# Kernel tuning notes

Hardware: AMD Instinct MI355X
Metric: run time of the kernel (lower is better)

The kernel has to match this reference:

```python
import jax, jax.numpy as jnp
import numpy as np

D = 1024            # BIGNET_DIM
GS = 16             # group_size
NG = D * D // GS    # groups per layer = 65536
N_LAYERS = 18       # 6 blocks * 3 linears
LORA_LAYERS = {0: 0, 6: 1, 12: 2}  # linear index -> lora slot (first linear of blocks 0,2,4)
RANK = 32
BATCH = 16384
EPS = 1e-5


def setup_inputs() -> dict:
    key = jax.random.key(0)
    ks = jax.random.split(key, 6)
    x = jax.random.normal(ks[0], (BATCH, D), dtype=jnp.float32)
    w_q = jax.random.randint(ks[1], (N_LAYERS, NG, GS), 0, 16, dtype=jnp.int32)
    w_norm = jax.random.uniform(ks[2], (N_LAYERS, NG, 1), dtype=jnp.float32)
    bias = jax.random.normal(ks[3], (N_LAYERS, D), dtype=jnp.float32) * 0.02
    lora_a = jax.random.normal(ks[4], (3, RANK, D), dtype=jnp.float32) * (1.0 / np.sqrt(D))
    lora_b = jax.random.normal(ks[5], (3, D, RANK), dtype=jnp.float32) * 0.02
    ln_w = jnp.ones((6, D), dtype=jnp.float32)
    ln_b = jnp.zeros((6, D), dtype=jnp.float32)
    return {"x": x, "w_q": w_q, "w_norm": w_norm, "bias": bias,
            "lora_a": lora_a, "lora_b": lora_b, "ln_w": ln_w, "ln_b": ln_b}


def _dequant(q, n):
    # block_dequantize_4bit: codes in [0,15] -> [-norm, +norm] per group
    return ((q.astype(jnp.float32) / 15.0) * 2.0 - 1.0) * n  # [NG, GS]


def reference(x, w_q, w_norm, bias, lora_a, lora_b, ln_w, ln_b):
    h = x
    for blk in range(6):
        for pos in range(3):
            l = blk * 3 + pos
            W = _dequant(w_q[l], w_norm[l]).reshape(D, D)  # [out, in]
            out = h @ W.T + bias[l]
            if l in LORA_LAYERS:
                i = LORA_LAYERS[l]
                out = out + (h @ lora_a[i].T) @ lora_b[i].T
            if pos < 2:
                out = jax.nn.relu(out)
            h = out
        mu = jnp.mean(h, axis=-1, keepdims=True)
        var = jnp.mean(jnp.square(h - mu), axis=-1, keepdims=True)
        h = (h - mu) * jax.lax.rsqrt(var + EPS) * ln_w[blk] + ln_b[blk]
    return h
```

## Files before the change

kernel.cpp:

```cpp
#include <hip/hip_runtime.h>
#include <cstdint>
#include <cstddef>


typedef short  bf16x8 __attribute__((ext_vector_type(8)));
typedef float  f32x4  __attribute__((ext_vector_type(4)));

__device__ __forceinline__ unsigned short f2bf(float f) {
  unsigned int u = __builtin_bit_cast(unsigned int, f);
  u += 0x7FFFu + ((u >> 16) & 1u);
  return (unsigned short)(u >> 16);
}

__device__ __forceinline__ void async_copy16(void* lds, const void* g) {
  __builtin_amdgcn_global_load_lds(
      (const __attribute__((address_space(1))) void*)(uintptr_t)(g),
      (__attribute__((address_space(3))) void*)(unsigned int)(uintptr_t)(lds),
      16, 0, 0);
}

__global__ __launch_bounds__(256) void dequant_kernel(
    const int* __restrict__ wq, const float* __restrict__ wn,
    const float* __restrict__ lora_a, const float* __restrict__ lora_b,
    unsigned short* __restrict__ Wbf) {
  const int l   = blockIdx.y;
  const int t   = threadIdx.x;
  const int blk = blockIdx.x;
  const long base = (long)l * 1048576;
  const float s = 2.0f / 15.0f;

  int4  q[4];
  float nrm[4];
#pragma unroll
  for (int k = 0; k < 4; ++k) {
    const int i4 = blk * 1024 + k * 256 + t;
    q[k]   = *(const int4*)(wq + base + (long)i4 * 4);
    nrm[k] = wn[l * 65536 + (i4 >> 2)];
  }

  float v[4][4];
#pragma unroll
  for (int k = 0; k < 4; ++k) {
    v[k][0] = ((float)q[k].x * s - 1.0f) * nrm[k];
    v[k][1] = ((float)q[k].y * s - 1.0f) * nrm[k];
    v[k][2] = ((float)q[k].z * s - 1.0f) * nrm[k];
    v[k][3] = ((float)q[k].w * s - 1.0f) * nrm[k];
  }

  const int slot = (l == 0) ? 0 : (l == 6) ? 1 : (l == 12) ? 2 : -1;
  if (slot >= 0) {
    const float* A = lora_a + slot * 32768 + t * 4;
    const float* B = lora_b + slot * 32768 + blk * 128;
#pragma unroll 8
    for (int r = 0; r < 32; ++r) {
      const float4 a4 = *(const float4*)(A + r * 1024);
#pragma unroll
      for (int k = 0; k < 4; ++k) {
        const float br = B[k * 32 + r];
        v[k][0] = fmaf(br, a4.x, v[k][0]);
        v[k][1] = fmaf(br, a4.y, v[k][1]);
        v[k][2] = fmaf(br, a4.z, v[k][2]);
        v[k][3] = fmaf(br, a4.w, v[k][3]);
      }
    }
  }

#pragma unroll
  for (int k = 0; k < 4; ++k) {
    unsigned short u[4] = {f2bf(v[k][0]), f2bf(v[k][1]),
                           f2bf(v[k][2]), f2bf(v[k][3])};
    const long e0 = base + ((long)blk * 1024 + k * 256 + t) * 4;
    *(uint2*)(Wbf + e0) = *(uint2*)u;
  }
}

__global__ __launch_bounds__(256) void cvt_bf16_kernel(
    const float* __restrict__ in, unsigned short* __restrict__ out) {
  const long b0 = (long)blockIdx.x * 4096 + threadIdx.x * 4;
  float4 v[4];
#pragma unroll
  for (int k = 0; k < 4; ++k) v[k] = *(const float4*)(in + b0 + k * 1024);
#pragma unroll
  for (int k = 0; k < 4; ++k) {
    unsigned short u[4] = {f2bf(v[k].x), f2bf(v[k].y), f2bf(v[k].z), f2bf(v[k].w)};
    *(ushort4*)(out + b0 + k * 1024) = *(ushort4*)u;
  }
}

template <int MODE>
__global__ __launch_bounds__(256, 4) void gemm_kernel(
    const unsigned short* __restrict__ H,
    const unsigned short* __restrict__ W,
    const float* __restrict__ bias,
    unsigned short* __restrict__ outb,
    float* __restrict__ outf) {
  constexpr int K = 1024;
  constexpr int NN = 1024;

  __shared__ uint4 ldsq[2048];
  char* base = (char*)ldsq;

  const int tid = threadIdx.x;
  const int w   = tid >> 6;
  const int ln  = tid & 63;
  const int b   = blockIdx.x;
  const int m0  = ((b & 7) * 16 + (b >> 6)) * 128;
  const int n0  = ((b >> 3) & 7) * 128;

  const int gc = (ln & 7) ^ (ln >> 3);
  const unsigned short* gA = H + (size_t)(m0 + w * 32 + (ln >> 3)) * K + gc * 8;
  const unsigned short* gB = W + (size_t)(n0 + w * 32 + (ln >> 3)) * K + gc * 8;
  char* ldsA = base + w * 4096;
  char* ldsB = base + 16384 + w * 4096;

  const int quad = ln >> 4;
  const int lrow = ln & 15;
  const int sw   = lrow & 7;
  const int c0   = ((quad)     ^ sw) * 16;
  const int c1   = ((quad + 4) ^ sw) * 16;
  const int wm   = (w >> 1) * 64;
  const int wn   = (w & 1) * 64;
  const char* fragA = base + (wm + lrow) * 128;
  const char* fragB = base + 16384 + (wn + lrow) * 128;

  f32x4 acc[4][4];
#pragma unroll
  for (int i = 0; i < 4; ++i)
#pragma unroll
    for (int j = 0; j < 4; ++j) acc[i][j] = (f32x4){0.f, 0.f, 0.f, 0.f};

  for (int kt = 0; kt < 16; ++kt) {
    const unsigned short* pA = gA + kt * 64;
    const unsigned short* pB = gB + kt * 64;
#pragma unroll
    for (int i = 0; i < 4; ++i) {
      async_copy16(ldsA + i * 1024, pA + (size_t)i * 8 * K);
      async_copy16(ldsB + i * 1024, pB + (size_t)i * 8 * K);
    }
    __syncthreads();
#pragma unroll
    for (int kk = 0; kk < 2; ++kk) {
      const int co = kk ? c1 : c0;
      bf16x8 af[4], bg[4];
#pragma unroll
      for (int mt = 0; mt < 4; ++mt)
        af[mt] = *(const bf16x8*)(fragA + mt * 2048 + co);
#pragma unroll
      for (int nt = 0; nt < 4; ++nt)
        bg[nt] = *(const bf16x8*)(fragB + nt * 2048 + co);
#pragma unroll
      for (int mt = 0; mt < 4; ++mt)
#pragma unroll
        for (int nt = 0; nt < 4; ++nt)
          acc[mt][nt] = __builtin_amdgcn_mfma_f32_16x16x32_bf16(
              af[mt], bg[nt], acc[mt][nt], 0, 0, 0);
    }
    __syncthreads();
  }

#pragma unroll
  for (int nt = 0; nt < 4; ++nt) {
    const int n = n0 + wn + nt * 16 + lrow;
    const float bs = bias[n];
#pragma unroll
    for (int mt = 0; mt < 4; ++mt) {
      const int mb = m0 + wm + mt * 16 + quad * 4;
      f32x4 v = acc[mt][nt];
#pragma unroll
      for (int r = 0; r < 4; ++r) {
        float o = v[r] + bs;
        if (MODE == 0) {
          o = fmaxf(o, 0.0f);
          outb[(size_t)(mb + r) * NN + n] = f2bf(o);
        } else {
          outf[(size_t)(mb + r) * NN + n] = o;
        }
      }
    }
  }
}

__global__ __launch_bounds__(256) void ln_kernel(
    const float* __restrict__ in, const float* __restrict__ lnw,
    const float* __restrict__ lnb, unsigned short* __restrict__ outb,
    float* __restrict__ outf, int wf32) {
  const int wv = threadIdx.x >> 6;
  const int ln = threadIdx.x & 63;
  const int row = blockIdx.x * 4 + wv;
  const float* p = in + (size_t)row * 1024;

  float4 v[4];
  float s = 0.f, q = 0.f;
#pragma unroll
  for (int c = 0; c < 4; ++c) {
    v[c] = *(const float4*)(p + c * 256 + ln * 4);
    s += v[c].x + v[c].y + v[c].z + v[c].w;
    q += v[c].x * v[c].x + v[c].y * v[c].y + v[c].z * v[c].z + v[c].w * v[c].w;
  }
#pragma unroll
  for (int off = 32; off; off >>= 1) {
    s += __shfl_xor(s, off);
    q += __shfl_xor(q, off);
  }
  const float mu  = s * (1.0f / 1024.0f);
  const float var = q * (1.0f / 1024.0f) - mu * mu;
  const float rs  = rsqrtf(var + 1e-5f);

#pragma unroll
  for (int c = 0; c < 4; ++c) {
    const int col = c * 256 + ln * 4;
    const float4 w4 = *(const float4*)(lnw + col);
    const float4 b4 = *(const float4*)(lnb + col);
    const float y0 = (v[c].x - mu) * rs * w4.x + b4.x;
    const float y1 = (v[c].y - mu) * rs * w4.y + b4.y;
    const float y2 = (v[c].z - mu) * rs * w4.z + b4.z;
    const float y3 = (v[c].w - mu) * rs * w4.w + b4.w;
    unsigned short u[4] = {f2bf(y0), f2bf(y1), f2bf(y2), f2bf(y3)};
    *(ushort4*)(outb + (size_t)row * 1024 + col) = *(ushort4*)u;
    if (wf32) {
      float4 y = make_float4(y0, y1, y2, y3);
      *(float4*)(outf + (size_t)row * 1024 + col) = y;
    }
  }
}

extern "C" void kernel_launch(void* const* d_in, const int* in_sizes, int n_in,
                              void* d_out, int out_size, void* d_ws, size_t ws_size,
                              hipStream_t stream) {
  const float* x    = (const float*)d_in[0];
  const int*   wq   = (const int*)d_in[1];
  const float* wn   = (const float*)d_in[2];
  const float* bias = (const float*)d_in[3];
  const float* la   = (const float*)d_in[4];
  const float* lb   = (const float*)d_in[5];
  const float* lnw  = (const float*)d_in[6];
  const float* lnb  = (const float*)d_in[7];
  float* out = (float*)d_out;

  char* ws = (char*)d_ws;
  unsigned short* Wbf = (unsigned short*)ws;
  unsigned short* hA  = (unsigned short*)(ws + 37748736);
  unsigned short* hB  = (unsigned short*)(ws + 37748736 + 33554432);

  dequant_kernel<<<dim3(256, 18), 256, 0, stream>>>(wq, wn, la, lb, Wbf);
  cvt_bf16_kernel<<<4096, 256, 0, stream>>>(x, hA);

  for (int blk = 0; blk < 6; ++blk) {
    const int l = blk * 3;
    gemm_kernel<0><<<1024, 256, 0, stream>>>(
        hA, Wbf + (size_t)l * 1048576, bias + l * 1024, hB, nullptr);
    gemm_kernel<0><<<1024, 256, 0, stream>>>(
        hB, Wbf + (size_t)(l + 1) * 1048576, bias + (l + 1) * 1024, hA, nullptr);
    gemm_kernel<1><<<1024, 256, 0, stream>>>(
        hA, Wbf + (size_t)(l + 2) * 1048576, bias + (l + 2) * 1024, nullptr, out);
    ln_kernel<<<4096, 256, 0, stream>>>(
        out, lnw + blk * 1024, lnb + blk * 1024, hA, out, blk == 5 ? 1 : 0);
  }
}
```

Measured before the change: 968.6 us.

## Replace GEMM with 256x256-tile, 8-wave, double-buffered pipelined kernel

Rewrites the bf16 GEMM to use 256x256 output tiles per 512-thread block, with a 128KB dynamic LDS double buffer. Global-to-LDS async copies for the next K tiles are interleaved with MFMA sub-blocks, using explicit vmcnt/lgkmcnt waits, barriers and setprio. The aim is to hide memory latency and raise operand reuse per LDS load. In exchange it uses only 256 blocks, which may underfill the GPU's CUs, and it relies on hand-tuned waitcnt sequencing that is fragile.

```diff
diff --git a/kernel.cpp b/kernel.cpp
--- a/kernel.cpp
+++ b/kernel.cpp
@@ -88,92 +88,161 @@
 }
 
 template <int MODE>
-__global__ __launch_bounds__(256, 4) void gemm_kernel(
+__global__ __launch_bounds__(512, 2) void gemm8_kernel(
     const unsigned short* __restrict__ H,
     const unsigned short* __restrict__ W,
     const float* __restrict__ bias,
     unsigned short* __restrict__ outb,
     float* __restrict__ outf) {
-  constexpr int K = 1024;
-  constexpr int NN = 1024;
-
-  __shared__ uint4 ldsq[2048];
-  char* base = (char*)ldsq;
+  extern __shared__ char smem[];
 
   const int tid = threadIdx.x;
   const int w   = tid >> 6;
   const int ln  = tid & 63;
-  const int b   = blockIdx.x;
-  const int m0  = ((b & 7) * 16 + (b >> 6)) * 128;
-  const int n0  = ((b >> 3) & 7) * 128;
-
-  const int gc = (ln & 7) ^ (ln >> 3);
-  const unsigned short* gA = H + (size_t)(m0 + w * 32 + (ln >> 3)) * K + gc * 8;
-  const unsigned short* gB = W + (size_t)(n0 + w * 32 + (ln >> 3)) * K + gc * 8;
-  char* ldsA = base + w * 4096;
-  char* ldsB = base + 16384 + w * 4096;
+  const int wm  = w >> 2;
+  const int wn  = w & 3;
+
+  const int b  = blockIdx.x;
+  const int s  = (b & 7) * 32 + (b >> 3);
+  const int m0 = (s >> 2) * 256;
+  const int n0 = (s & 3) * 256;
+
+  const int gc    = (ln & 7) ^ ((ln >> 3) & 7);
+  const int rowst = w * 8 + (ln >> 3);
+  const unsigned eA = (unsigned)(m0 + rowst) * 1024u + gc * 8;
+  const unsigned eB = (unsigned)(n0 + rowst) * 1024u + gc * 8;
+  const int wofs = w * 1024;
 
   const int quad = ln >> 4;
   const int lrow = ln & 15;
   const int sw   = lrow & 7;
   const int c0   = ((quad)     ^ sw) * 16;
   const int c1   = ((quad + 4) ^ sw) * 16;
-  const int wm   = (w >> 1) * 64;
-  const int wn   = (w & 1) * 64;
-  const char* fragA = base + (wm + lrow) * 128;
-  const char* fragB = base + 16384 + (wn + lrow) * 128;
-
-  f32x4 acc[4][4];
-#pragma unroll
-  for (int i = 0; i < 4; ++i)
+  const int aoff = (wm * 128 + lrow) * 128;
+  const int boff = (wn * 64  + lrow) * 128;
+
+#define STAGE_A(T_, D_, F_, J_)                                                \
+  async_copy16(smem + (D_) * 65536 + (F_) * 16384 + (J_) * 8192 + wofs,        \
+               H + eA + (unsigned)((T_) * 64 + ((F_) * 128 + (J_) * 64) * 1024))
+#define STAGE_B(T_, D_, F_, J_)                                                \
+  async_copy16(smem + (D_) * 65536 + 32768 + (F_) * 16384 + (J_) * 8192 + wofs,\
+               W + eB + (unsigned)((T_) * 64 + ((F_) * 128 + (J_) * 64) * 1024))
+#define MM16(AV, BV, I0, J0)                                                   \
+  {                                                                            \
+    _Pragma("unroll") for (int i_ = 0; i_ < 4; ++i_) {                         \
+      _Pragma("unroll") for (int j_ = 0; j_ < 2; ++j_) {                       \
+        acc[(I0) + i_][(J0) + j_] = __builtin_amdgcn_mfma_f32_16x16x32_bf16(   \
+            AV[i_][0], BV[j_][0], acc[(I0) + i_][(J0) + j_], 0, 0, 0);         \
+        acc[(I0) + i_][(J0) + j_] = __builtin_amdgcn_mfma_f32_16x16x32_bf16(   \
+            AV[i_][1], BV[j_][1], acc[(I0) + i_][(J0) + j_], 0, 0, 0);         \
+      }                                                                        \
+    }                                                                          \
+  }
+#define LDSUB4(DST, BASE, OFF)                                                 \
+  {                                                                            \
+    _Pragma("unroll") for (int i_ = 0; i_ < 4; ++i_) {                         \
+      DST[i_][0] = *(const bf16x8*)((BASE) + (OFF) + i_ * 2048 + c0);          \
+      DST[i_][1] = *(const bf16x8*)((BASE) + (OFF) + i_ * 2048 + c1);          \
+    }                                                                          \
+  }
+#define LDSUB2(DST, BASE, OFF)                                                 \
+  {                                                                            \
+    _Pragma("unroll") for (int j_ = 0; j_ < 2; ++j_) {                         \
+      DST[j_][0] = *(const bf16x8*)((BASE) + (OFF) + j_ * 2048 + c0);          \
+      DST[j_][1] = *(const bf16x8*)((BASE) + (OFF) + j_ * 2048 + c1);          \
+    }                                                                          \
+  }
+
+  f32x4 acc[8][4];
+#pragma unroll
+  for (int i = 0; i < 8; ++i)
 #pragma unroll
     for (int j = 0; j < 4; ++j) acc[i][j] = (f32x4){0.f, 0.f, 0.f, 0.f};
 
+  STAGE_A(0, 0, 0, 0); STAGE_A(0, 0, 0, 1);
+  STAGE_A(0, 0, 1, 0); STAGE_A(0, 0, 1, 1);
+  STAGE_B(0, 0, 0, 0); STAGE_B(0, 0, 0, 1);
+  STAGE_B(0, 0, 1, 0); STAGE_B(0, 0, 1, 1);
+  asm volatile("" ::: "memory");
+  STAGE_A(1, 1, 0, 0); STAGE_A(1, 1, 0, 1);
+  STAGE_A(1, 1, 1, 0); STAGE_A(1, 1, 1, 1);
+  asm volatile("s_waitcnt vmcnt(4)" ::: "memory");
+  __builtin_amdgcn_s_barrier();
+
+  bf16x8 a0[4][2], a1[4][2], bb[2][2];
+
+#pragma unroll 2
   for (int kt = 0; kt < 16; ++kt) {
-    const unsigned short* pA = gA + kt * 64;
-    const unsigned short* pB = gB + kt * 64;
-#pragma unroll
-    for (int i = 0; i < 4; ++i) {
-      async_copy16(ldsA + i * 1024, pA + (size_t)i * 8 * K);
-      async_copy16(ldsB + i * 1024, pB + (size_t)i * 8 * K);
+    const int BUF = kt & 1;
+    const char* At = smem + BUF * 65536;
+    const char* Bt = At + 32768;
+    const int  nb = BUF ^ 1;
+    const bool ib = (kt < 15);
+    const bool ia = (kt < 14);
+
+    LDSUB4(a0, At, aoff);
+    LDSUB2(bb, Bt, boff);
+    if (ib) { STAGE_B(kt + 1, nb, 0, 0); STAGE_B(kt + 1, nb, 0, 1); }
+    __builtin_amdgcn_s_barrier();
+    asm volatile("s_waitcnt lgkmcnt(0)" ::: "memory");
+    __builtin_amdgcn_s_setprio(1);
+    MM16(a0, bb, 0, 0);
+    __builtin_amdgcn_s_setprio(0);
+    __builtin_amdgcn_s_barrier();
+
+    LDSUB4(a1, At, aoff + 8192);
+    if (ib) { STAGE_B(kt + 1, nb, 1, 0); STAGE_B(kt + 1, nb, 1, 1); }
+    __builtin_amdgcn_s_barrier();
+    asm volatile("s_waitcnt lgkmcnt(0)" ::: "memory");
+    __builtin_amdgcn_s_setprio(1);
+    MM16(a1, bb, 4, 0);
+    __builtin_amdgcn_s_setprio(0);
+    __builtin_amdgcn_s_barrier();
+
+    LDSUB2(bb, Bt, boff + 4096);
+    if (ia) { STAGE_A(kt + 2, BUF, 0, 0); STAGE_A(kt + 2, BUF, 0, 1); }
+    __builtin_amdgcn_s_barrier();
+    asm volatile("s_waitcnt lgkmcnt(0)" ::: "memory");
+    __builtin_amdgcn_s_setprio(1);
+    MM16(a1, bb, 4, 2);
+    __builtin_amdgcn_s_setprio(0);
+    __builtin_amdgcn_s_barrier();
+
+    if (ia) { STAGE_A(kt + 2, BUF, 1, 0); STAGE_A(kt + 2, BUF, 1, 1); }
+    __builtin_amdgcn_s_barrier();
+    __builtin_amdgcn_s_setprio(1);
+    MM16(a0, bb, 0, 2);
+    __builtin_amdgcn_s_setprio(0);
+    if (kt < 14) {
+      asm volatile("s_waitcnt vmcnt(4)" ::: "memory");
+    } else if (kt == 14) {
+      asm volatile("s_waitcnt vmcnt(0)" ::: "memory");
     }
-    __syncthreads();
-#pragma unroll
-    for (int kk = 0; kk < 2; ++kk) {
-      const int co = kk ? c1 : c0;
-      bf16x8 af[4], bg[4];
-#pragma unroll
-      for (int mt = 0; mt < 4; ++mt)
-        af[mt] = *(const bf16x8*)(fragA + mt * 2048 + co);
-#pragma unroll
-      for (int nt = 0; nt < 4; ++nt)
-        bg[nt] = *(const bf16x8*)(fragB + nt * 2048 + co);
-#pragma unroll
-      for (int mt = 0; mt < 4; ++mt)
-#pragma unroll
-        for (int nt = 0; nt < 4; ++nt)
-          acc[mt][nt] = __builtin_amdgcn_mfma_f32_16x16x32_bf16(
-              af[mt], bg[nt], acc[mt][nt], 0, 0, 0);
-    }
-    __syncthreads();
-  }
+    __builtin_amdgcn_s_barrier();
+  }
+
+#undef LDSUB2
+#undef LDSUB4
+#undef MM16
+#undef STAGE_B
+#undef STAGE_A
 
 #pragma unroll
   for (int nt = 0; nt < 4; ++nt) {
-    const int n = n0 + wn + nt * 16 + lrow;
+    const int n = n0 + wn * 64 + nt * 16 + lrow;
     const float bs = bias[n];
 #pragma unroll
-    for (int mt = 0; mt < 4; ++mt) {
-      const int mb = m0 + wm + mt * 16 + quad * 4;
-      f32x4 v = acc[mt][nt];
+    for (int mt = 0; mt < 8; ++mt) {
+      const int mb = m0 + wm * 128 + mt * 16 + quad * 4;
+      const f32x4 v = acc[mt][nt];
 #pragma unroll
       for (int r = 0; r < 4; ++r) {
         float o = v[r] + bs;
         if (MODE == 0) {
           o = fmaxf(o, 0.0f);
-          outb[(size_t)(mb + r) * NN + n] = f2bf(o);
+          outb[(size_t)(mb + r) * 1024 + n] = f2bf(o);
         } else {
-          outf[(size_t)(mb + r) * NN + n] = o;
+          outf[(size_t)(mb + r) * 1024 + n] = o;
         }
       }
     }
@@ -247,11 +316,11 @@
 
   for (int blk = 0; blk < 6; ++blk) {
     const int l = blk * 3;
-    gemm_kernel<0><<<1024, 256, 0, stream>>>(
+    gemm8_kernel<0><<<256, 512, 131072, stream>>>(
         hA, Wbf + (size_t)l * 1048576, bias + l * 1024, hB, nullptr);
-    gemm_kernel<0><<<1024, 256, 0, stream>>>(
+    gemm8_kernel<0><<<256, 512, 131072, stream>>>(
         hB, Wbf + (size_t)(l + 1) * 1048576, bias + (l + 1) * 1024, hA, nullptr);
-    gemm_kernel<1><<<1024, 256, 0, stream>>>(
+    gemm8_kernel<1><<<256, 512, 131072, stream>>>(
         hA, Wbf + (size_t)(l + 2) * 1048576, bias + (l + 2) * 1024, nullptr, out);
     ln_kernel<<<4096, 256, 0, stream>>>(
         out, lnw + blk * 1024, lnb + blk * 1024, hA, out, blk == 5 ? 1 : 0);
```

Measured after the change: 985.0 us. About the same (+1.7%).
